# Kernel optimization log

Measured on AMD Instinct MI355X. Metric: run time of the kernel, lower is better.

## Reference

```python
import jax, jax.numpy as jnp
import numpy as np

B, L, D, H = 4, 2048, 512, 8
HD = D // H
NEG = -1e9


def setup_inputs() -> dict:
    key = jax.random.key(0)
    ks = jax.random.split(key, 11)
    s = 1.0 / np.sqrt(D)
    inp = {
        "q": jax.random.normal(ks[0], (B, L, D), jnp.float32),
        "k": jax.random.normal(ks[1], (B, L, D), jnp.float32),
        "v": jax.random.normal(ks[2], (B, L, D), jnp.float32),
        "mask": jnp.broadcast_to(jnp.tril(jnp.ones((L, L), jnp.int32)), (B, L, L)),
        "Wq": jax.random.normal(ks[3], (D, D), jnp.float32) * s,
        "bq": jax.random.normal(ks[4], (D,), jnp.float32) * s,
        "Wk": jax.random.normal(ks[5], (D, D), jnp.float32) * s,
        "bk": jax.random.normal(ks[6], (D,), jnp.float32) * s,
        "Wv": jax.random.normal(ks[7], (D, D), jnp.float32) * s,
        "bv": jax.random.normal(ks[8], (D,), jnp.float32) * s,
        "Wo": jax.random.normal(ks[9], (D, D), jnp.float32) * s,
        "bo": jax.random.normal(ks[10], (D,), jnp.float32) * s,
    }
    return inp


def reference(q, k, v, mask, Wq, bq, Wk, bk, Wv, bv, Wo, bo):
    # Linear projections (torch Linear: x @ W.T + b)
    Q = (q @ Wq.T + bq).reshape(B, L, H, HD).transpose(0, 2, 1, 3)  # [B,H,L,hd]
    K = (k @ Wk.T + bk).reshape(B, L, H, HD).transpose(0, 2, 1, 3)
    V = (v @ Wv.T + bv).reshape(B, L, H, HD).transpose(0, 2, 1, 3)
    # scaled dot-product attention with masked_fill(mask==0, -1e9)
    score = jnp.einsum('bhqd,bhkd->bhqk', Q, K) / jnp.sqrt(jnp.float32(HD))
    score = jnp.where(mask[:, None, :, :] == 0, NEG, score)
    attn = jax.nn.softmax(score, axis=-1)
    ctx = jnp.einsum('bhqk,bhkd->bhqd', attn, V)  # [B,H,L,hd]
    ctx = ctx.transpose(0, 2, 1, 3).reshape(B, L, D)
    return ctx @ Wo.T + bo
```

## Files before the change

kernel.cpp:

```cpp
#include <hip/hip_runtime.h>
#include <hip/hip_bf16.h>
#include <math.h>

constexpr int Bc  = 4;
constexpr int Lc  = 2048;
constexpr int Dc  = 512;
constexpr int Hc  = 8;
constexpr int HDc = 64;

constexpr int GK = Dc;
constexpr int BK = 64;

typedef __attribute__((ext_vector_type(8))) short bf16x8;
typedef __attribute__((ext_vector_type(4))) float f32x4;

static __device__ __forceinline__ short f2bf(float x) {
    __hip_bfloat16 h = __float2bfloat16(x);
    return (short)__builtin_bit_cast(unsigned short, h);
}

static __device__ __forceinline__ void gload_lds16(const void* g, void* l) {
    __builtin_amdgcn_global_load_lds(
        (const __attribute__((address_space(1))) void*)g,
        (__attribute__((address_space(3))) void*)l, 16, 0, 0);
}

__global__ __launch_bounds__(256)
void cast_all(const float* __restrict__ q, const float* __restrict__ k,
              const float* __restrict__ v, const float* __restrict__ wq,
              const float* __restrict__ wk, const float* __restrict__ wv,
              const float* __restrict__ wo, short* __restrict__ dst) {
    const size_t i = ((size_t)blockIdx.x * 256 + threadIdx.x) * 8;
    const float* src; size_t off;
    if      (i <  4194304) { src = q;  off = i; }
    else if (i <  8388608) { src = k;  off = i -  4194304; }
    else if (i < 12582912) { src = v;  off = i -  8388608; }
    else if (i < 12845056) { src = wq; off = i - 12582912; }
    else if (i < 13107200) { src = wk; off = i - 12845056; }
    else if (i < 13369344) { src = wv; off = i - 13107200; }
    else                   { src = wo; off = i - 13369344; }
    const float4 a = *(const float4*)(src + off);
    const float4 b = *(const float4*)(src + off + 4);
    bf16x8 o;
    o[0] = f2bf(a.x); o[1] = f2bf(a.y); o[2] = f2bf(a.z); o[3] = f2bf(a.w);
    o[4] = f2bf(b.x); o[5] = f2bf(b.y); o[6] = f2bf(b.z); o[7] = f2bf(b.w);
    *(bf16x8*)(dst + i) = o;
}

template<int BM, int BN, int WMT, int WNT>
__device__ __forceinline__ void gemm_tile(const short* __restrict__ A,
                                          const short* __restrict__ W,
                                          short* As, short* Bs,
                                          f32x4 (&acc)[WMT][WNT],
                                          int m0, int n0) {
    const int tid  = threadIdx.x;
    const int w    = tid >> 6;
    const int lane = tid & 63;
    const int low4 = lane & 15;
    const int quad = lane >> 4;
    const int wm   = w & 1, wn = w >> 1;
    const int lrow = lane >> 3;
    const int lchk = (lane & 7) * 8;

    for (int k0 = 0; k0 < GK; k0 += BK) {
#pragma unroll
        for (int i = 0; i < BM / 32; ++i) {
            const int r0 = i * 32 + w * 8;
            gload_lds16(A + (size_t)(m0 + r0 + lrow) * GK + k0 + lchk, As + r0 * BK);
        }
#pragma unroll
        for (int i = 0; i < BN / 32; ++i) {
            const int r0 = i * 32 + w * 8;
            gload_lds16(W + (size_t)(n0 + r0 + lrow) * GK + k0 + lchk, Bs + r0 * BK);
        }
        __syncthreads();
#pragma unroll
        for (int ks = 0; ks < 2; ++ks) {
            bf16x8 af[WMT], bfr[WNT];
#pragma unroll
            for (int mi = 0; mi < WMT; ++mi)
                af[mi] = *(const bf16x8*)(As + (wm * WMT * 16 + mi * 16 + low4) * BK + ks * 32 + quad * 8);
#pragma unroll
            for (int ni = 0; ni < WNT; ++ni)
                bfr[ni] = *(const bf16x8*)(Bs + (wn * WNT * 16 + ni * 16 + low4) * BK + ks * 32 + quad * 8);
#pragma unroll
            for (int mi = 0; mi < WMT; ++mi)
#pragma unroll
                for (int ni = 0; ni < WNT; ++ni)
                    acc[mi][ni] = __builtin_amdgcn_mfma_f32_16x16x32_bf16(af[mi], bfr[ni], acc[mi][ni], 0, 0, 0);
        }
        __syncthreads();
    }
}

__global__ __launch_bounds__(256)
void qkv_gemm(const short* __restrict__ Xq, const short* __restrict__ Xk,
              const short* __restrict__ Xv, const short* __restrict__ Wcat,
              const float* __restrict__ bq, const float* __restrict__ bk,
              const float* __restrict__ bv,
              short* __restrict__ Qw, short* __restrict__ Kw, short* __restrict__ Vw) {
    __shared__ __align__(16) short Smem[128 * 138];
    short* As = Smem;
    short* Bs = Smem + 8192;
    short* Ts = Smem;

    const int tid = threadIdx.x;
    const int i    = blockIdx.x;
    const int slot = i >> 3;
    const int g    = (i & 7) + 8 * (slot >> 2);
    const int j    = slot & 3;
    const int z    = g >> 6;
    const int m0   = (g & 63) * 128;
    const int n0   = z * 512 + j * 128;

    const short* A    = (z == 0) ? Xq : (z == 1) ? Xk : Xv;
    const float* bias = (z == 0) ? bq : (z == 1) ? bk : bv;

    f32x4 acc[4][4];
#pragma unroll
    for (int mi = 0; mi < 4; ++mi)
#pragma unroll
        for (int ni = 0; ni < 4; ++ni) acc[mi][ni] = (f32x4){0.f, 0.f, 0.f, 0.f};

    gemm_tile<128, 128, 4, 4>(A, Wcat, As, Bs, acc, m0, n0);

    const int lane = tid & 63, w = tid >> 6;
    const int low4 = lane & 15, quad = lane >> 4;
    const int wm = w & 1, wn = w >> 1;

    if (z < 2) {
        short* Y = (z == 0) ? Qw : Kw;
#pragma unroll
        for (int mi = 0; mi < 4; ++mi)
#pragma unroll
            for (int ni = 0; ni < 4; ++ni)
#pragma unroll
                for (int r = 0; r < 4; ++r) {
                    const int rowL = wm * 64 + mi * 16 + quad * 4 + r;
                    const int colL = wn * 64 + ni * 16 + low4;
                    const int c    = (n0 & 511) + colL;
                    Ts[rowL * 138 + colL] = f2bf(acc[mi][ni][r] + bias[c]);
                }
        __syncthreads();
        const int jj = tid & 7;
        const int b = m0 >> 11;
#pragma unroll
        for (int it = 0; it < 8; ++it) {
            const int slot2 = it * 32 + (tid >> 3);
            const int row  = slot2 >> 1, half = slot2 & 1;
            const int c0 = (n0 & 511) + half * 64;
            const int h  = c0 >> 6;
            const int l  = (m0 & 2047) + row;
            short* dst = Y + (((size_t)b * Hc + h) * Lc + l) * HDc + jj * 8;
            *(bf16x8*)dst = *(const bf16x8*)(Ts + row * 138 + half * 64 + jj * 8);
        }
    } else {
#pragma unroll
        for (int mi = 0; mi < 4; ++mi)
#pragma unroll
            for (int ni = 0; ni < 4; ++ni)
#pragma unroll
                for (int r = 0; r < 4; ++r) {
                    const int rowL = wm * 64 + mi * 16 + quad * 4 + r;
                    const int colL = wn * 64 + ni * 16 + low4;
                    const int c    = (n0 + colL) & 511;
                    Ts[colL * 136 + rowL] = f2bf(acc[mi][ni][r] + bias[c]);
                }
        __syncthreads();
        const int hdl = tid >> 1, seg = tid & 1;
        const int c  = (n0 + hdl) & 511;
        const int h  = c >> 6, hd = c & 63;
        const int b  = m0 >> 11, l0 = (m0 & 2047) + seg * 64;
        short* dst = Vw + (((size_t)b * Hc + h) * HDc + hd) * Lc + l0;
        const short* srcT = Ts + hdl * 136 + seg * 64;
#pragma unroll
        for (int jj = 0; jj < 8; ++jj)
            *(bf16x8*)(dst + jj * 8) = *(const bf16x8*)(srcT + jj * 8);
    }
}

__global__ __launch_bounds__(256)
void out_gemm(const short* __restrict__ A, const short* __restrict__ W,
              const float* __restrict__ bias, float* __restrict__ Y) {
    __shared__ __align__(16) float SmemF[64 * 132];
    short* As = (short*)SmemF;
    short* Bs = As + 64 * BK;
    float* Tf = SmemF;

    const int tid = threadIdx.x;
    const int i    = blockIdx.x;
    const int slot = i >> 3;
    const int g    = (i & 7) + 8 * (slot >> 2);
    const int j    = slot & 3;
    const int m0   = g * 64;
    const int n0   = j * 128;

    f32x4 acc[2][4];
#pragma unroll
    for (int mi = 0; mi < 2; ++mi)
#pragma unroll
        for (int ni = 0; ni < 4; ++ni) acc[mi][ni] = (f32x4){0.f, 0.f, 0.f, 0.f};

    gemm_tile<64, 128, 2, 4>(A, W, As, Bs, acc, m0, n0);

    const int lane = tid & 63, w = tid >> 6;
    const int low4 = lane & 15, quad = lane >> 4;
    const int wm = w & 1, wn = w >> 1;
#pragma unroll
    for (int mi = 0; mi < 2; ++mi)
#pragma unroll
        for (int ni = 0; ni < 4; ++ni)
#pragma unroll
            for (int r = 0; r < 4; ++r) {
                const int rowL = wm * 32 + mi * 16 + quad * 4 + r;
                const int colL = wn * 64 + ni * 16 + low4;
                Tf[rowL * 132 + colL] = acc[mi][ni][r] + bias[n0 + colL];
            }
    __syncthreads();

    const int c = (tid & 31) * 4;
#pragma unroll
    for (int p = 0; p < 8; ++p) {
        const int row = p * 8 + (tid >> 5);
        *(float4*)(Y + (size_t)(m0 + row) * Dc + n0 + c) =
            *(const float4*)(Tf + row * 132 + c);
    }
}

__global__ __launch_bounds__(256)
void flash_attn(const short* __restrict__ Qb, const short* __restrict__ Kb,
                const short* __restrict__ VTb, short* __restrict__ ctx) {
    __shared__ __align__(16) short Kf[2][4096];
    __shared__ __align__(16) short Vf[2][4096];
    __shared__ __align__(16) short Ps[4][16 * 72];

    const int tid  = threadIdx.x;
    const int w    = tid >> 6;
    const int lane = tid & 63;
    const int low4 = lane & 15;
    const int quad = lane >> 4;

    const int bh = blockIdx.x & 31;
    const int qt = 31 - (blockIdx.x >> 5);
    const int q0w = qt * 64 + w * 16;

    const short* Qg = Qb  + (size_t)bh * Lc * HDc;
    const short* Kg = Kb  + (size_t)bh * Lc * HDc;
    const short* Vg = VTb + (size_t)bh * HDc * Lc;

    const bf16x8 qa0 = *(const bf16x8*)(Qg + (size_t)(q0w + low4) * HDc + quad * 8);
    const bf16x8 qa1 = *(const bf16x8*)(Qg + (size_t)(q0w + low4) * HDc + 32 + quad * 8);

    f32x4 o[4];
    float lp[4] = {0.f, 0.f, 0.f, 0.f};
#pragma unroll
    for (int i = 0; i < 4; ++i) o[i] = (f32x4){0.f, 0.f, 0.f, 0.f};

    const float C8 = 0.18033688f;

#define STAGE(KT_, BUF_)                                                        \
    {                                                                           \
        _Pragma("unroll")                                                       \
        for (int p = 0; p < 2; ++p) {                                           \
            const int dc = w + 4 * p;                                           \
            gload_lds16(Kg + (size_t)((KT_) + lane) * HDc + dc * 8,             \
                        &Kf[BUF_][(dc * 64 + lane) * 8]);                       \
            gload_lds16(Vg + (size_t)lane * Lc + (KT_) + dc * 8,                \
                        &Vf[BUF_][(dc * 64 + lane) * 8]);                       \
        }                                                                       \
    }

    STAGE(0, 0);
    __syncthreads();

    for (int t = 0; t <= qt; ++t) {
        const int buf = t & 1;
        if (t < qt) STAGE((t + 1) * 64, buf ^ 1);

        f32x4 s[4];
#pragma unroll
        for (int nt = 0; nt < 4; ++nt) s[nt] = (f32x4){0.f, 0.f, 0.f, 0.f};
#pragma unroll
        for (int ks = 0; ks < 2; ++ks) {
            const bf16x8 qa = ks ? qa1 : qa0;
#pragma unroll
            for (int nt = 0; nt < 4; ++nt) {
                const bf16x8 kf = *(const bf16x8*)(&Kf[buf][((ks * 4 + quad) * 64 + nt * 16 + low4) * 8]);
                s[nt] = __builtin_amdgcn_mfma_f32_16x16x32_bf16(qa, kf, s[nt], 0, 0, 0);
            }
        }

        short* pw = Ps[w];
        const int kt = t * 64;
        if (t < qt) {
#pragma unroll
            for (int nt = 0; nt < 4; ++nt)
#pragma unroll
                for (int r = 0; r < 4; ++r) {
                    const float p = exp2f(s[nt][r] * C8);
                    lp[r] += p;
                    pw[(quad * 4 + r) * 72 + nt * 16 + low4] = f2bf(p);
                }
        } else {
#pragma unroll
            for (int nt = 0; nt < 4; ++nt)
#pragma unroll
                for (int r = 0; r < 4; ++r) {
                    const int qrow = q0w + quad * 4 + r;
                    const int col  = kt + nt * 16 + low4;
                    float p = exp2f(s[nt][r] * C8);
                    if (col > qrow) p = 0.f;
                    lp[r] += p;
                    pw[(quad * 4 + r) * 72 + nt * 16 + low4] = f2bf(p);
                }
        }

        __asm__ volatile("s_waitcnt lgkmcnt(0)" ::: "memory");

#pragma unroll
        for (int ks = 0; ks < 2; ++ks) {
            const bf16x8 pf = *(const bf16x8*)(pw + low4 * 72 + ks * 32 + quad * 8);
#pragma unroll
            for (int nt = 0; nt < 4; ++nt) {
                const bf16x8 vf = *(const bf16x8*)(&Vf[buf][((ks * 4 + quad) * 64 + nt * 16 + low4) * 8]);
                o[nt] = __builtin_amdgcn_mfma_f32_16x16x32_bf16(pf, vf, o[nt], 0, 0, 0);
            }
        }

        __syncthreads();
    }

#pragma unroll
    for (int off = 1; off < 16; off <<= 1)
#pragma unroll
        for (int r = 0; r < 4; ++r)
            lp[r] += __shfl_xor(lp[r], off, 64);

    const int b = bh >> 3, h = bh & 7;
#pragma unroll
    for (int r = 0; r < 4; ++r) {
        const float inv = 1.f / lp[r];
        const int q = q0w + quad * 4 + r;
#pragma unroll
        for (int nt = 0; nt < 4; ++nt)
            ctx[(size_t)(b * Lc + q) * Dc + h * HDc + nt * 16 + low4] = f2bf(o[nt][r] * inv);
    }
#undef STAGE
}

extern "C" void kernel_launch(void* const* d_in, const int* in_sizes, int n_in,
                              void* d_out, int out_size, void* d_ws, size_t ws_size,
                              hipStream_t stream) {
    const float* q  = (const float*)d_in[0];
    const float* k  = (const float*)d_in[1];
    const float* v  = (const float*)d_in[2];
    const float* Wq = (const float*)d_in[4];
    const float* bq = (const float*)d_in[5];
    const float* Wk = (const float*)d_in[6];
    const float* bk = (const float*)d_in[7];
    const float* Wv = (const float*)d_in[8];
    const float* bv = (const float*)d_in[9];
    const float* Wo = (const float*)d_in[10];
    const float* bo = (const float*)d_in[11];
    float* out = (float*)d_out;

    const size_t per = (size_t)Bc * Lc * Dc;
    const size_t wsz = (size_t)Dc * Dc;
    short* Xq   = (short*)d_ws;
    short* Xk   = Xq + per;
    short* Xv   = Xk + per;
    short* Wcat = Xv + per;
    short* Wob  = Wcat + 3 * wsz;
    short* Qw   = Wob + wsz;
    short* Kw   = Qw + per;
    short* Vw   = Kw + per;
    short* Cw   = Vw + per;

    cast_all<<<6656, 256, 0, stream>>>(q, k, v, Wq, Wk, Wv, Wo, Xq);

    qkv_gemm<<<768, 256, 0, stream>>>(Xq, Xk, Xv, Wcat,
                                      bq, bk, bv, Qw, Kw, Vw);

    flash_attn<<<1024, 256, 0, stream>>>(Qw, Kw, Vw, Cw);

    out_gemm<<<512, 256, 0, stream>>>(Cw, Wob, bo, out);
}
```

Measured before the change: 237.1 us.

## Restructure flash attention with 32x32 MFMA, register-resident P, and triple-buffered staging

Rewrites the attention kernel to use 128-row query tiles (32 rows per wave) with 32x32x16 bf16 MFMAs, computing S transposed so the probabilities stay in registers. They are packed with v_cvt_pk_bf16 and v_permlane32_swap instead of being round-tripped through LDS. K/V staging becomes triple-buffered with an XOR-swizzled LDS layout and explicit vmcnt waits. Blocks are reordered to balance causal work, and fully masked tiles are skipped per wave. The aim is to cut LDS traffic, sync overhead and bank conflicts, at the cost of halving the grid to 512 blocks and higher register pressure.

After: 238.0 us. About the same (+0.4%).

```diff
diff --git a/kernel.cpp b/kernel.cpp
--- a/kernel.cpp
+++ b/kernel.cpp
@@ -12,11 +12,20 @@
 constexpr int BK = 64;
 
 typedef __attribute__((ext_vector_type(8))) short bf16x8;
+typedef __attribute__((ext_vector_type(4))) short bf16x4;
 typedef __attribute__((ext_vector_type(4))) float f32x4;
+typedef __attribute__((ext_vector_type(16))) float f32x16;
+typedef __attribute__((ext_vector_type(4))) int i32x4;
 
 static __device__ __forceinline__ short f2bf(float x) {
     __hip_bfloat16 h = __float2bfloat16(x);
     return (short)__builtin_bit_cast(unsigned short, h);
+}
+
+static __device__ __forceinline__ int cvtpk_bf16(float lo, float hi) {
+    int r;
+    asm("v_cvt_pk_bf16_f32 %0, %1, %2" : "=v"(r) : "v"(lo), "v"(hi));
+    return r;
 }
 
 static __device__ __forceinline__ void gload_lds16(const void* g, void* l) {
@@ -227,123 +236,148 @@
     }
 }
 
-__global__ __launch_bounds__(256)
+__global__ __launch_bounds__(256, 2)
 void flash_attn(const short* __restrict__ Qb, const short* __restrict__ Kb,
                 const short* __restrict__ VTb, short* __restrict__ ctx) {
-    __shared__ __align__(16) short Kf[2][4096];
-    __shared__ __align__(16) short Vf[2][4096];
-    __shared__ __align__(16) short Ps[4][16 * 72];
+    __shared__ __align__(16) short Kf[3][4096];
+    __shared__ __align__(16) short Vf[3][4096];
 
     const int tid  = threadIdx.x;
     const int w    = tid >> 6;
     const int lane = tid & 63;
-    const int low4 = lane & 15;
-    const int quad = lane >> 4;
-
-    const int bh = blockIdx.x & 31;
-    const int qt = 31 - (blockIdx.x >> 5);
-    const int q0w = qt * 64 + w * 16;
+    const int t31  = lane & 31;
+    const int hh   = lane >> 5;
+    const int x7   = t31 & 7;
+
+    const int u  = blockIdx.x;
+    const int bh = u & 31;
+    const int m  = (u < 256) ? (u >> 5) : (15 - ((u - 256) >> 5));
+    const int nt = 2 * m + 2;
+    const int q0w = m * 128 + w * 32;
 
     const short* Qg = Qb  + (size_t)bh * Lc * HDc;
     const short* Kg = Kb  + (size_t)bh * Lc * HDc;
     const short* Vg = VTb + (size_t)bh * HDc * Lc;
 
-    const bf16x8 qa0 = *(const bf16x8*)(Qg + (size_t)(q0w + low4) * HDc + quad * 8);
-    const bf16x8 qa1 = *(const bf16x8*)(Qg + (size_t)(q0w + low4) * HDc + 32 + quad * 8);
-
-    f32x4 o[4];
-    float lp[4] = {0.f, 0.f, 0.f, 0.f};
-#pragma unroll
-    for (int i = 0; i < 4; ++i) o[i] = (f32x4){0.f, 0.f, 0.f, 0.f};
+    bf16x8 qa[4];
+#pragma unroll
+    for (int hc = 0; hc < 4; ++hc)
+        qa[hc] = *(const bf16x8*)(Qg + (size_t)(q0w + t31) * HDc + hc * 16 + hh * 8);
+#pragma unroll
+    for (int hc = 0; hc < 4; ++hc)
+        asm volatile("" :: "v"(qa[hc]));
+
+    const int grow = lane >> 3;
+    const int gcol = ((lane & 7) ^ grow) * 8;
+
+#define STAGE(KT_, BUF_)                                                       \
+    {                                                                          \
+        _Pragma("unroll")                                                      \
+        for (int p = 0; p < 2; ++p) {                                          \
+            const int ii = w + 4 * p;                                          \
+            gload_lds16(Kg + (size_t)((KT_) + ii * 8 + grow) * HDc + gcol,     \
+                        &Kf[BUF_][ii * 512]);                                  \
+            gload_lds16(Vg + (size_t)(ii * 8 + grow) * Lc + (KT_) + gcol,      \
+                        &Vf[BUF_][ii * 512]);                                  \
+        }                                                                      \
+    }
+
+    STAGE(0, 0);
+    STAGE(64, 1);
+    asm volatile("s_waitcnt vmcnt(4)" ::: "memory");
+    __builtin_amdgcn_sched_barrier(0);
+    __builtin_amdgcn_s_barrier();
+
+    f32x16 o0, o1;
+#pragma unroll
+    for (int i = 0; i < 16; ++i) { o0[i] = 0.f; o1[i] = 0.f; }
+    float lps = 0.f;
 
     const float C8 = 0.18033688f;
-
-#define STAGE(KT_, BUF_)                                                        \
-    {                                                                           \
-        _Pragma("unroll")                                                       \
-        for (int p = 0; p < 2; ++p) {                                           \
-            const int dc = w + 4 * p;                                           \
-            gload_lds16(Kg + (size_t)((KT_) + lane) * HDc + dc * 8,             \
-                        &Kf[BUF_][(dc * 64 + lane) * 8]);                       \
-            gload_lds16(Vg + (size_t)lane * Lc + (KT_) + dc * 8,                \
-                        &Vf[BUF_][(dc * 64 + lane) * 8]);                       \
-        }                                                                       \
-    }
-
-    STAGE(0, 0);
-    __syncthreads();
-
-    for (int t = 0; t <= qt; ++t) {
-        const int buf = t & 1;
-        if (t < qt) STAGE((t + 1) * 64, buf ^ 1);
-
-        f32x4 s[4];
-#pragma unroll
-        for (int nt = 0; nt < 4; ++nt) s[nt] = (f32x4){0.f, 0.f, 0.f, 0.f};
-#pragma unroll
-        for (int ks = 0; ks < 2; ++ks) {
-            const bf16x8 qa = ks ? qa1 : qa0;
-#pragma unroll
-            for (int nt = 0; nt < 4; ++nt) {
-                const bf16x8 kf = *(const bf16x8*)(&Kf[buf][((ks * 4 + quad) * 64 + nt * 16 + low4) * 8]);
-                s[nt] = __builtin_amdgcn_mfma_f32_16x16x32_bf16(qa, kf, s[nt], 0, 0, 0);
+    int br = 0;
+
+    for (int t = 0; t < nt; ++t) {
+        const int kt = t * 64;
+        const int bs = (br + 2 >= 3) ? br - 1 : br + 2;
+        if (t + 2 < nt) STAGE(kt + 128, bs);
+
+        if (kt <= q0w + 31) {
+            f32x16 s0, s1;
+#pragma unroll
+            for (int i = 0; i < 16; ++i) { s0[i] = 0.f; s1[i] = 0.f; }
+            const short* kfb = Kf[br];
+#pragma unroll
+            for (int hc = 0; hc < 4; ++hc) {
+                const int cb = ((hc * 2 + hh) ^ x7) << 3;
+                const bf16x8 k0 = *(const bf16x8*)(kfb + t31 * 64 + cb);
+                const bf16x8 k1 = *(const bf16x8*)(kfb + (32 + t31) * 64 + cb);
+                s0 = __builtin_amdgcn_mfma_f32_32x32x16_bf16(k0, qa[hc], s0, 0, 0, 0);
+                s1 = __builtin_amdgcn_mfma_f32_32x32x16_bf16(k1, qa[hc], s1, 0, 0, 0);
+            }
+
+            if (kt + 63 <= q0w) {
+#pragma unroll
+                for (int r = 0; r < 16; ++r) {
+                    const float p0 = exp2f(s0[r] * C8);
+                    const float p1 = exp2f(s1[r] * C8);
+                    lps += p0 + p1; s0[r] = p0; s1[r] = p1;
+                }
+            } else {
+                const int qv = q0w + t31;
+                const int kb0 = kt + 4 * hh;
+#pragma unroll
+                for (int r = 0; r < 16; ++r) {
+                    const int kl = kb0 + (r & 3) + 8 * (r >> 2);
+                    const float p0 = (kl      <= qv) ? exp2f(s0[r] * C8) : 0.f;
+                    const float p1 = (kl + 32 <= qv) ? exp2f(s1[r] * C8) : 0.f;
+                    lps += p0 + p1; s0[r] = p0; s1[r] = p1;
+                }
+            }
+
+            const short* vfb = Vf[br];
+#pragma unroll
+            for (int kc = 0; kc < 4; ++kc) {
+                const int g = 8 * (kc & 1);
+                float e0, e1, e2, e3, e4, e5, e6, e7;
+                if (kc < 2) { e0=s0[g]; e1=s0[g+1]; e2=s0[g+2]; e3=s0[g+3];
+                              e4=s0[g+4]; e5=s0[g+5]; e6=s0[g+6]; e7=s0[g+7]; }
+                else        { e0=s1[g]; e1=s1[g+1]; e2=s1[g+2]; e3=s1[g+3];
+                              e4=s1[g+4]; e5=s1[g+5]; e6=s1[g+6]; e7=s1[g+7]; }
+                int u0 = cvtpk_bf16(e0, e1);
+                int u1 = cvtpk_bf16(e2, e3);
+                int v0 = cvtpk_bf16(e4, e5);
+                int v1 = cvtpk_bf16(e6, e7);
+                asm volatile("v_permlane32_swap_b32 %0, %1" : "+v"(u0), "+v"(v0));
+                asm volatile("v_permlane32_swap_b32 %0, %1" : "+v"(u1), "+v"(v1));
+                i32x4 pw; pw[0] = u0; pw[1] = u1; pw[2] = v0; pw[3] = v1;
+                const bf16x8 pa = __builtin_bit_cast(bf16x8, pw);
+
+                const int cb = ((kc * 2 + hh) ^ x7) << 3;
+                const bf16x8 vf0 = *(const bf16x8*)(vfb + t31 * 64 + cb);
+                const bf16x8 vf1 = *(const bf16x8*)(vfb + (32 + t31) * 64 + cb);
+                o0 = __builtin_amdgcn_mfma_f32_32x32x16_bf16(pa, vf0, o0, 0, 0, 0);
+                o1 = __builtin_amdgcn_mfma_f32_32x32x16_bf16(pa, vf1, o1, 0, 0, 0);
             }
         }
 
-        short* pw = Ps[w];
-        const int kt = t * 64;
-        if (t < qt) {
-#pragma unroll
-            for (int nt = 0; nt < 4; ++nt)
-#pragma unroll
-                for (int r = 0; r < 4; ++r) {
-                    const float p = exp2f(s[nt][r] * C8);
-                    lp[r] += p;
-                    pw[(quad * 4 + r) * 72 + nt * 16 + low4] = f2bf(p);
-                }
-        } else {
-#pragma unroll
-            for (int nt = 0; nt < 4; ++nt)
-#pragma unroll
-                for (int r = 0; r < 4; ++r) {
-                    const int qrow = q0w + quad * 4 + r;
-                    const int col  = kt + nt * 16 + low4;
-                    float p = exp2f(s[nt][r] * C8);
-                    if (col > qrow) p = 0.f;
-                    lp[r] += p;
-                    pw[(quad * 4 + r) * 72 + nt * 16 + low4] = f2bf(p);
-                }
-        }
-
-        __asm__ volatile("s_waitcnt lgkmcnt(0)" ::: "memory");
-
-#pragma unroll
-        for (int ks = 0; ks < 2; ++ks) {
-            const bf16x8 pf = *(const bf16x8*)(pw + low4 * 72 + ks * 32 + quad * 8);
-#pragma unroll
-            for (int nt = 0; nt < 4; ++nt) {
-                const bf16x8 vf = *(const bf16x8*)(&Vf[buf][((ks * 4 + quad) * 64 + nt * 16 + low4) * 8]);
-                o[nt] = __builtin_amdgcn_mfma_f32_16x16x32_bf16(pf, vf, o[nt], 0, 0, 0);
-            }
-        }
-
-        __syncthreads();
-    }
-
-#pragma unroll
-    for (int off = 1; off < 16; off <<= 1)
-#pragma unroll
-        for (int r = 0; r < 4; ++r)
-            lp[r] += __shfl_xor(lp[r], off, 64);
-
-    const int b = bh >> 3, h = bh & 7;
-#pragma unroll
-    for (int r = 0; r < 4; ++r) {
-        const float inv = 1.f / lp[r];
-        const int q = q0w + quad * 4 + r;
-#pragma unroll
-        for (int nt = 0; nt < 4; ++nt)
-            ctx[(size_t)(b * Lc + q) * Dc + h * HDc + nt * 16 + low4] = f2bf(o[nt][r] * inv);
+        if (t + 2 < nt) asm volatile("s_waitcnt vmcnt(4)" ::: "memory");
+        else            asm volatile("s_waitcnt vmcnt(0)" ::: "memory");
+        __builtin_amdgcn_sched_barrier(0);
+        __builtin_amdgcn_s_barrier();
+        br = (br + 1 >= 3) ? 0 : br + 1;
+    }
+
+    lps += __shfl_xor(lps, 32, 64);
+    const float inv = 1.f / lps;
+    const int b = bh >> 3, head = bh & 7;
+    short* cg = ctx + (size_t)b * Lc * Dc + (size_t)head * HDc;
+#pragma unroll
+    for (int r = 0; r < 16; ++r) {
+        const int qloc = (r & 3) + 8 * (r >> 2) + 4 * hh;
+        const float iq = __shfl(inv, qloc, 64);
+        short* row = cg + (size_t)(q0w + qloc) * Dc;
+        row[t31]      = f2bf(o0[r] * iq);
+        row[32 + t31] = f2bf(o1[r] * iq);
     }
 #undef STAGE
 }
@@ -381,7 +415,7 @@
     qkv_gemm<<<768, 256, 0, stream>>>(Xq, Xk, Xv, Wcat,
                                       bq, bk, bv, Qw, Kw, Vw);
 
-    flash_attn<<<1024, 256, 0, stream>>>(Qw, Kw, Vw, Cw);
+    flash_attn<<<512, 256, 0, stream>>>(Qw, Kw, Vw, Cw);
 
     out_gemm<<<512, 256, 0, stream>>>(Cw, Wob, bo, out);
 }
```
